# Kernel tuning notes

Hardware: AMD Instinct MI355X
Metric: run time of the kernel (lower is better)

Reference implementation:

```python
import jax, jax.numpy as jnp
import numpy as np

N_OSC = 256
N_LAYERS = 4
STEPS = 10
DT = 0.1
B = 1024
D_IN = 512
D_OUT = 128


def setup_inputs() -> dict:
    key = jax.random.key(0)
    ks = jax.random.split(key, 12)
    n = N_OSC

    def rn(k, shape, s=1.0):
        return jax.random.normal(k, shape, jnp.float32) * s

    K = rn(ks[0], (N_LAYERS, n, n), 0.1)
    K = (K + jnp.swapaxes(K, -1, -2)) / 2  # symmetric init as in torch
    return {
        "x": rn(ks[1], (B, D_IN)),
        "enc_W1": rn(ks[2], (D_IN, 2 * n), 0.02), "enc_b1": jnp.zeros((2 * n,), jnp.float32),
        "enc_W2": rn(ks[3], (2 * n, n), 0.02), "enc_b2": jnp.zeros((n,), jnp.float32),
        "K": K,
        "omega": rn(ks[4], (N_LAYERS, n), 0.1),
        "K_global": jnp.full((N_LAYERS,), 0.5, jnp.float32),
        "op_strength": jnp.full((6,), 0.5, jnp.float32),
        "exchange_logits": rn(ks[5], (n, n), 0.1),
        "catalyze_freq": rn(ks[6], (n,), 0.1),
        "sel_W1": rn(ks[7], (n + 2, 64), 0.05), "sel_b1": jnp.zeros((64,), jnp.float32),
        "sel_W2": rn(ks[8], (64, 6), 0.05), "sel_b2": jnp.zeros((6,), jnp.float32),
        "dec_W1": rn(ks[9], (2 * n, 2 * D_OUT), 0.02), "dec_b1": jnp.zeros((2 * D_OUT,), jnp.float32),
        "dec_W2": rn(ks[10], (2 * D_OUT, D_OUT), 0.02), "dec_b2": jnp.zeros((D_OUT,), jnp.float32),
        "z_momentum": jnp.float32(0.1),
        "z_decay": jnp.float32(0.05),
    }


def _kuramoto_layer(theta, K, omega, K_global):
    n = theta.shape[-1]

    def step(th, _):
        diff = th[:, None, :] - th[:, :, None]          # [B, i, j] = theta_j - theta_i
        coupling = jnp.sum(K * jnp.sin(diff), axis=-1)  # reduce over j -> [B, n]
        th_new = th + DT * (omega + (K_global / n) * coupling)
        th_new = jnp.arctan2(jnp.sin(th_new), jnp.cos(th_new))  # wrap to (-pi, pi]
        return th_new, None

    theta, _ = jax.lax.scan(jax.checkpoint(step), theta, None, length=STEPS)
    cm = jnp.mean(jnp.cos(theta), axis=-1)
    sm = jnp.mean(jnp.sin(theta), axis=-1)
    return theta, jnp.sqrt(cm * cm + sm * sm)  # Kuramoto order parameter r


def _soft_permutation(logits):
    P = logits
    for _ in range(5):  # Sinkhorn normalization in log space
        P = P - jax.nn.logsumexp(P, axis=-1, keepdims=True)
        P = P - jax.nn.logsumexp(P, axis=-2, keepdims=True)
    return jnp.exp(P)


def _forward(x, enc_W1, enc_b1, enc_W2, enc_b2, K, omega, K_global,
             op_strength, exchange_logits, catalyze_freq,
             sel_W1, sel_b1, sel_W2, sel_b2, dec_W1, dec_b1, dec_W2, dec_b2,
             z_momentum, z_decay):
    n = N_OSC
    # input encoding -> initial phases in (-pi, pi)
    h = jax.nn.gelu(x @ enc_W1 + enc_b1, approximate=False)
    theta = jnp.tanh(h @ enc_W2 + enc_b2) * jnp.pi

    z = jnp.float32(0.1)
    P = _soft_permutation(exchange_logits)
    k_mult = jnp.float32(1.0)              # AMPLIFY/CONTAIN carry to next layer
    om_add = jnp.zeros((n,), theta.dtype)  # CATALYZE carry to next layer

    for li in range(N_LAYERS):
        theta, r = _kuramoto_layer(theta, K[li] * k_mult, omega[li] + om_add, K_global[li])
        # z-coordinate attractor update: dz = mom*(r_mean - z) - decay*(z - 0.5)
        dz = z_momentum * (jnp.mean(r) - z) - z_decay * (z - 0.5)
        z = jnp.clip(z + 0.01 * dz, 0.0, 1.0)
        # APL operator selection from [theta, coherence, z]
        feat = jnp.concatenate(
            [theta, r[:, None], jnp.broadcast_to(z, (theta.shape[0], 1))], axis=-1)
        logits = jax.nn.gelu(feat @ sel_W1 + sel_b1, approximate=False) @ sel_W2 + sel_b2
        op = jnp.argmax(jnp.mean(logits, axis=0))
        strength = op_strength[op] * r[:, None]  # coherence-modulated strength
        sm_ = jnp.mean(strength)
        # apply operator: phase mods now, K/omega mods carried into next layer
        noise = jax.random.normal(jax.random.fold_in(jax.random.key(42), li),
                                  theta.shape, theta.dtype)
        theta = jnp.where(op == 3, theta @ P,                                # EXCHANGE
                          jnp.where(op == 4, theta + noise * strength * 0.2,  # INHIBIT
                                    theta))
        k_mult = jnp.where(op == 1, 1.0 + sm_ * 0.5,        # AMPLIFY
                           jnp.where(op == 2, 1.0 - sm_ * 0.3, 1.0))  # CONTAIN
        om_add = jnp.where(op == 5, catalyze_freq * sm_,    # CATALYZE
                           jnp.zeros_like(catalyze_freq))

    # decode from (cos, sin) phase embedding
    emb = jnp.concatenate([jnp.cos(theta), jnp.sin(theta)], axis=-1)  # [B, 2n]
    out = jax.nn.gelu(emb @ dec_W1 + dec_b1, approximate=False) @ dec_W2 + dec_b2
    return out


def reference(x, enc_W1, enc_b1, enc_W2, enc_b2, K, omega, K_global,
              op_strength, exchange_logits, catalyze_freq,
              sel_W1, sel_b1, sel_W2, sel_b2, dec_W1, dec_b1, dec_W2, dec_b2,
              z_momentum, z_decay):
    return _forward(x, enc_W1, enc_b1, enc_W2, enc_b2, K, omega, K_global,
                    op_strength, exchange_logits, catalyze_freq,
                    sel_W1, sel_b1, sel_W2, sel_b2, dec_W1, dec_b1, dec_W2, dec_b2,
                    z_momentum, z_decay)
```

## Files before the change

### kernel.cpp

```cpp
#include <hip/hip_runtime.h>
#include <hip/hip_fp16.h>
#include <math.h>

#define DT_F 0.1f

#define SC_Z     0
#define SC_RMEAN 1
#define SC_KMULT 2
#define SC_OP    3
#define SC_OPSTR 4
#define SC_SM    5

typedef __attribute__((ext_vector_type(8))) short short8;
typedef __attribute__((ext_vector_type(4))) float f32x4;


__device__ __forceinline__ float gelu_f(float x) {
    return 0.5f * x * (1.0f + erff(x * 0.7071067811865475f));
}

__device__ __forceinline__ unsigned short f2bf_rne(float f) {
    union { float f; unsigned u; } v; v.f = f;
    unsigned x = v.u;
    unsigned r = x + 0x7fffu + ((x >> 16) & 1u);
    return (unsigned short)(r >> 16);
}

__device__ __forceinline__ unsigned rotl32(unsigned v, int d) {
    return (v << d) | (v >> (32 - d));
}

__device__ __forceinline__ void threefry2x32(unsigned k0, unsigned k1,
                                             unsigned x0, unsigned x1,
                                             unsigned& o0, unsigned& o1) {
    unsigned k2 = k0 ^ k1 ^ 0x1BD11BDAu;
    x0 += k0; x1 += k1;
    const int r0[4] = {13, 15, 26, 6};
    const int r1[4] = {17, 29, 16, 24};
#pragma unroll
    for (int g = 0; g < 5; ++g) {
        const int* R = (g & 1) ? r1 : r0;
#pragma unroll
        for (int q = 0; q < 4; ++q) { x0 += x1; x1 = rotl32(x1, R[q]); x1 ^= x0; }
        unsigned a, b;
        switch (g) {
            case 0:  a = k1; b = k2 + 1u; break;
            case 1:  a = k2; b = k0 + 2u; break;
            case 2:  a = k0; b = k1 + 3u; break;
            case 3:  a = k1; b = k2 + 4u; break;
            default: a = k2; b = k0 + 5u; break;
        }
        x0 += a; x1 += b;
    }
    o0 = x0; o1 = x1;
}

__device__ __forceinline__ float erfinv_xla(float x) {
    float w = -log1pf(-x * x);
    float p;
    if (w < 5.0f) {
        w -= 2.5f;
        p = 2.81022636e-08f;
        p = fmaf(p, w, 3.43273939e-07f);
        p = fmaf(p, w, -3.5233877e-06f);
        p = fmaf(p, w, -4.39150654e-06f);
        p = fmaf(p, w, 0.00021858087f);
        p = fmaf(p, w, -0.00125372503f);
        p = fmaf(p, w, -0.00417768164f);
        p = fmaf(p, w, 0.246640727f);
        p = fmaf(p, w, 1.50140941f);
    } else {
        w = sqrtf(w) - 3.0f;
        p = -0.000200214257f;
        p = fmaf(p, w, 0.000100950558f);
        p = fmaf(p, w, 0.00134934322f);
        p = fmaf(p, w, -0.00367342844f);
        p = fmaf(p, w, 0.00573950773f);
        p = fmaf(p, w, -0.0076224613f);
        p = fmaf(p, w, 0.00943887047f);
        p = fmaf(p, w, 1.00167406f);
        p = fmaf(p, w, 2.83297682f);
    }
    return p * x;
}

__device__ __forceinline__ float jax_normal_elem(unsigned fk0, unsigned fk1, unsigned flat) {
    const unsigned HALF = 131072u;
    unsigned idx = (flat < HALF) ? flat : (flat - HALF);
    unsigned o0, o1;
    threefry2x32(fk0, fk1, idx, idx + HALF, o0, o1);
    unsigned bits = (flat < HALF) ? o0 : o1;
    float f = __uint_as_float((bits >> 9) | 0x3F800000u) - 1.0f;
    const float LO = __uint_as_float(0xBF7FFFFFu);
    float u = fmaxf(LO, fmaf(f, 2.0f, LO));
    return 1.41421356237f * erfinv_xla(u);
}


__global__ __launch_bounds__(256) void prep_wt_kernel(
    const float* __restrict__ W1, const float* __restrict__ W2,
    const float* __restrict__ W3, const float* __restrict__ W4,
    unsigned short* __restrict__ T1, unsigned short* __restrict__ T2,
    unsigned short* __restrict__ T3, unsigned short* __restrict__ T4)
{
    __shared__ float tile[64][65];
    int b = blockIdx.x;
    const float* W; unsigned short* T; int K, N, kt, nt;
    if (b < 64)       { W = W1; T = T1; K = 512; N = 512; kt = b >> 3; nt = b & 7; }
    else if (b < 96)  { b -= 64;  W = W2; T = T2; K = 512; N = 256; kt = b >> 2; nt = b & 3; }
    else if (b < 128) { b -= 96;  W = W3; T = T3; K = 512; N = 256; kt = b >> 2; nt = b & 3; }
    else              { b -= 128; W = W4; T = T4; K = 256; N = 128; kt = b >> 1; nt = b & 1; }
    const int k0 = kt * 64, n0 = nt * 64;
    const int t = threadIdx.x;

#pragma unroll
    for (int i = 0; i < 4; ++i) {
        int r = (t >> 4) + i * 16;
        int c = (t & 15) * 4;
        float4 v = *reinterpret_cast<const float4*>(&W[(k0 + r) * N + n0 + c]);
        tile[r][c] = v.x; tile[r][c + 1] = v.y; tile[r][c + 2] = v.z; tile[r][c + 3] = v.w;
    }
    __syncthreads();
#pragma unroll
    for (int i = 0; i < 4; ++i) {
        int nn = (t >> 4) + i * 16;
        int kc = (t & 15) * 4;
        ushort4 o;
        o.x = f2bf_rne(tile[kc + 0][nn]);
        o.y = f2bf_rne(tile[kc + 1][nn]);
        o.z = f2bf_rne(tile[kc + 2][nn]);
        o.w = f2bf_rne(tile[kc + 3][nn]);
        *reinterpret_cast<ushort4*>(&T[(n0 + nn) * K + k0 + kc]) = o;
    }
}


template <int ACT, int KF, bool EMB>
__global__ __launch_bounds__(256) void gemm_mfma_kernel(
    const float* __restrict__ A,
    const unsigned short* __restrict__ Wt,
    const float* __restrict__ bias,
    float* __restrict__ C, int N)
{
    constexpr int STR = KF + 8;
    __shared__ __align__(16) unsigned short A_s[64 * STR];
    __shared__ __align__(16) unsigned short B_s[64 * STR];
    const int tid = threadIdx.x;
    const int m_base = blockIdx.y * 64;
    const int n_base = blockIdx.x * 64;

    {
        constexpr int ITERS = 64 * KF / 2048;
#pragma unroll
        for (int c = 0; c < ITERS; ++c) {
            const int f = c * 2048 + tid * 8;
            const int row = f / KF, k = f % KF;
            float4 a0, a1;
            if (EMB) {
                const int kk = k & 255;
                a0 = *reinterpret_cast<const float4*>(&A[(m_base + row) * 256 + kk]);
                a1 = *reinterpret_cast<const float4*>(&A[(m_base + row) * 256 + kk + 4]);
                if (k < 256) {
                    a0.x = __cosf(a0.x); a0.y = __cosf(a0.y); a0.z = __cosf(a0.z); a0.w = __cosf(a0.w);
                    a1.x = __cosf(a1.x); a1.y = __cosf(a1.y); a1.z = __cosf(a1.z); a1.w = __cosf(a1.w);
                } else {
                    a0.x = __sinf(a0.x); a0.y = __sinf(a0.y); a0.z = __sinf(a0.z); a0.w = __sinf(a0.w);
                    a1.x = __sinf(a1.x); a1.y = __sinf(a1.y); a1.z = __sinf(a1.z); a1.w = __sinf(a1.w);
                }
            } else {
                a0 = *reinterpret_cast<const float4*>(&A[(m_base + row) * KF + k]);
                a1 = *reinterpret_cast<const float4*>(&A[(m_base + row) * KF + k + 4]);
            }
            short8 v;
            v[0] = (short)f2bf_rne(a0.x); v[1] = (short)f2bf_rne(a0.y);
            v[2] = (short)f2bf_rne(a0.z); v[3] = (short)f2bf_rne(a0.w);
            v[4] = (short)f2bf_rne(a1.x); v[5] = (short)f2bf_rne(a1.y);
            v[6] = (short)f2bf_rne(a1.z); v[7] = (short)f2bf_rne(a1.w);
            *reinterpret_cast<short8*>(&A_s[row * STR + k]) = v;
        }
    }
    {
        constexpr int ITERS = 64 * KF / 2048;
#pragma unroll
        for (int c = 0; c < ITERS; ++c) {
            const int f = c * 2048 + tid * 8;
            const int n = f / KF, k = f % KF;
            short8 v = *reinterpret_cast<const short8*>(&Wt[(n_base + n) * KF + k]);
            *reinterpret_cast<short8*>(&B_s[n * STR + k]) = v;
        }
    }
    __syncthreads();

    const int l = tid & 63, w = tid >> 6;
    const int lo = l & 15, hi = l >> 4;

    f32x4 acc0 = {0.f, 0.f, 0.f, 0.f};
    f32x4 acc1 = {0.f, 0.f, 0.f, 0.f};
    f32x4 acc2 = {0.f, 0.f, 0.f, 0.f};
    f32x4 acc3 = {0.f, 0.f, 0.f, 0.f};
#pragma unroll
    for (int kc = 0; kc < KF / 32; ++kc) {
        short8 af = *reinterpret_cast<const short8*>(&A_s[(w * 16 + lo) * STR + kc * 32 + hi * 8]);
        short8 b0 = *reinterpret_cast<const short8*>(&B_s[(0 * 16 + lo) * STR + kc * 32 + hi * 8]);
        short8 b1 = *reinterpret_cast<const short8*>(&B_s[(1 * 16 + lo) * STR + kc * 32 + hi * 8]);
        short8 b2 = *reinterpret_cast<const short8*>(&B_s[(2 * 16 + lo) * STR + kc * 32 + hi * 8]);
        short8 b3 = *reinterpret_cast<const short8*>(&B_s[(3 * 16 + lo) * STR + kc * 32 + hi * 8]);
        acc0 = __builtin_amdgcn_mfma_f32_16x16x32_bf16(af, b0, acc0, 0, 0, 0);
        acc1 = __builtin_amdgcn_mfma_f32_16x16x32_bf16(af, b1, acc1, 0, 0, 0);
        acc2 = __builtin_amdgcn_mfma_f32_16x16x32_bf16(af, b2, acc2, 0, 0, 0);
        acc3 = __builtin_amdgcn_mfma_f32_16x16x32_bf16(af, b3, acc3, 0, 0, 0);
    }

#pragma unroll
    for (int nf = 0; nf < 4; ++nf) {
        const f32x4 a = (nf == 0) ? acc0 : (nf == 1) ? acc1 : (nf == 2) ? acc2 : acc3;
        const int n = n_base + nf * 16 + lo;
        const float bv = bias[n];
#pragma unroll
        for (int q = 0; q < 4; ++q) {
            const int m = m_base + w * 16 + hi * 4 + q;
            float v = a[q] + bv;
            if (ACT == 1) v = gelu_f(v);
            else if (ACT == 2) v = tanhf(v) * 3.14159274101257324f;
            C[m * N + n] = v;
        }
    }
}


__global__ __launch_bounds__(1024) void sinkhorn_kernel(const float* __restrict__ logits,
                                                        float* __restrict__ P,
                                                        float* __restrict__ scal,
                                                        float* __restrict__ om_add) {
    __shared__ __align__(16) __half Eh[256][260];
    __shared__ float a[256], b[256];
    __shared__ float part[8][256];
    const int t = threadIdx.x;

    if (t < 8) {
        float val = 0.0f;
        if (t == SC_Z) val = 0.1f;
        if (t == SC_KMULT) val = 1.0f;
        scal[t] = val;
    }
    if (t < 256) { om_add[t] = 0.0f; b[t] = 1.0f; }

    {
        const int r = t >> 2, c0 = (t & 3) * 64;
#pragma unroll
        for (int j = 0; j < 64; j += 4) {
            float4 x4 = *reinterpret_cast<const float4*>(&logits[r * 256 + c0 + j]);
            __half2 h01 = __floats2half2_rn(__expf(x4.x), __expf(x4.y));
            __half2 h23 = __floats2half2_rn(__expf(x4.z), __expf(x4.w));
            *reinterpret_cast<__half2*>(&Eh[r][c0 + j])     = h01;
            *reinterpret_cast<__half2*>(&Eh[r][c0 + j + 2]) = h23;
        }
    }
    __syncthreads();

    for (int it = 0; it < 5; ++it) {
        {
            const int i = t & 255, q = t >> 8;
            float s0 = 0.f, s1 = 0.f, s2 = 0.f, s3 = 0.f;
#pragma unroll
            for (int j0 = 0; j0 < 64; j0 += 4) {
                float2 e4 = *reinterpret_cast<const float2*>(&Eh[i][q * 64 + j0]);
                const __half2* hp = reinterpret_cast<const __half2*>(&e4);
                float2 f01 = __half22float2(hp[0]);
                float2 f23 = __half22float2(hp[1]);
                float4 bv = *reinterpret_cast<const float4*>(&b[q * 64 + j0]);
                s0 = fmaf(f01.x, bv.x, s0);
                s1 = fmaf(f01.y, bv.y, s1);
                s2 = fmaf(f23.x, bv.z, s2);
                s3 = fmaf(f23.y, bv.w, s3);
            }
            part[q][i] = (s0 + s1) + (s2 + s3);
        }
        __syncthreads();
        if (t < 256) a[t] = 1.0f / (part[0][t] + part[1][t] + part[2][t] + part[3][t]);
        __syncthreads();
        {
            const int jp = t & 127, seg = t >> 7;
            float s0 = 0.f, s1 = 0.f;
#pragma unroll
            for (int i0 = 0; i0 < 32; i0 += 4) {
                float4 av = *reinterpret_cast<const float4*>(&a[seg * 32 + i0]);
                __half2 e0 = *reinterpret_cast<const __half2*>(&Eh[seg * 32 + i0 + 0][2 * jp]);
                __half2 e1 = *reinterpret_cast<const __half2*>(&Eh[seg * 32 + i0 + 1][2 * jp]);
                __half2 e2 = *reinterpret_cast<const __half2*>(&Eh[seg * 32 + i0 + 2][2 * jp]);
                __half2 e3 = *reinterpret_cast<const __half2*>(&Eh[seg * 32 + i0 + 3][2 * jp]);
                float2 f0 = __half22float2(e0), f1 = __half22float2(e1);
                float2 f2 = __half22float2(e2), f3 = __half22float2(e3);
                s0 = fmaf(f0.x, av.x, s0); s1 = fmaf(f0.y, av.x, s1);
                s0 = fmaf(f1.x, av.y, s0); s1 = fmaf(f1.y, av.y, s1);
                s0 = fmaf(f2.x, av.z, s0); s1 = fmaf(f2.y, av.z, s1);
                s0 = fmaf(f3.x, av.w, s0); s1 = fmaf(f3.y, av.w, s1);
            }
            part[seg][2 * jp]     = s0;
            part[seg][2 * jp + 1] = s1;
        }
        __syncthreads();
        if (t < 256) {
            float s = ((part[0][t] + part[1][t]) + (part[2][t] + part[3][t]))
                    + ((part[4][t] + part[5][t]) + (part[6][t] + part[7][t]));
            b[t] = 1.0f / s;
        }
        __syncthreads();
    }

    {
        const int r = t >> 2, c0 = (t & 3) * 64;
        const float ar = a[r];
#pragma unroll
        for (int j = 0; j < 64; j += 4) {
            float2 e4 = *reinterpret_cast<const float2*>(&Eh[r][c0 + j]);
            const __half2* hp = reinterpret_cast<const __half2*>(&e4);
            float2 f01 = __half22float2(hp[0]);
            float2 f23 = __half22float2(hp[1]);
            float4 bv = *reinterpret_cast<const float4*>(&b[c0 + j]);
            float4 o;
            o.x = f01.x * ar * bv.x;
            o.y = f01.y * ar * bv.y;
            o.z = f23.x * ar * bv.z;
            o.w = f23.y * ar * bv.w;
            *reinterpret_cast<float4*>(&P[r * 256 + c0 + j]) = o;
        }
    }
}


__global__ __launch_bounds__(512) void kuramoto_mfma_kernel(
    float* __restrict__ theta,
    const float* __restrict__ Kl,
    const float* __restrict__ omega_l,
    const float* __restrict__ Kg_p,
    const float* __restrict__ scal,
    const float* __restrict__ om_add,
    float* __restrict__ r_out,
    float* __restrict__ rpart,
    const float* __restrict__ P,
    int li)
{
    __shared__ __align__(16) unsigned short s_lds[16][264];
    __shared__ __align__(16) unsigned short c_lds[16][264];
    __shared__ __align__(16) float th_lds[16][260];
    __shared__ float rp_s[16][128];
    __shared__ float rp_c[16][128];
    __shared__ float red_s[16][32];
    __shared__ float red_c[16][32];
    __shared__ float rloc[16];

    const int tid = threadIdx.x;
    const int l  = tid & 63;
    const int w  = tid >> 6;
    const int lo = l & 15;
    const int hi = l >> 4;
    const int cb = w * 32;
    const int r0 = blockIdx.x * 16;

    const float gk = Kg_p[0] * (1.0f / 256.0f) * scal[SC_KMULT];
    const int op_prev = (int)scal[SC_OP];

    {
        const int row = tid >> 5;
        const int c0 = (tid & 31) * 8;
        float4 a = *reinterpret_cast<const float4*>(&theta[(r0 + row) * 256 + c0]);
        float4 b = *reinterpret_cast<const float4*>(&theta[(r0 + row) * 256 + c0 + 4]);
        *reinterpret_cast<float4*>(&th_lds[row][c0])     = a;
        *reinterpret_cast<float4*>(&th_lds[row][c0 + 4]) = b;
    }

    short8 kfrag[8][2];
#pragma unroll
    for (int nf = 0; nf < 2; ++nf) {
        const int col = cb + nf * 16 + lo;
        const float* krow = Kl + col * 256;
#pragma unroll
        for (int ks = 0; ks < 8; ++ks) {
            const int kb = ks * 32 + hi * 8;
            float4 k0 = *reinterpret_cast<const float4*>(&krow[kb]);
            float4 k1 = *reinterpret_cast<const float4*>(&krow[kb + 4]);
            short8 f;
            f[0] = (short)f2bf_rne(k0.x); f[1] = (short)f2bf_rne(k0.y);
            f[2] = (short)f2bf_rne(k0.z); f[3] = (short)f2bf_rne(k0.w);
            f[4] = (short)f2bf_rne(k1.x); f[5] = (short)f2bf_rne(k1.y);
            f[6] = (short)f2bf_rne(k1.z); f[7] = (short)f2bf_rne(k1.w);
            kfrag[ks][nf] = f;
        }
    }
    __syncthreads();

    float t[2][4];
    if (op_prev == 3) {
        float acc[2][4] = {};
        for (int j = 0; j < 256; ++j) {
            float p0 = P[j * 256 + cb + lo];
            float p1 = P[j * 256 + cb + 16 + lo];
#pragma unroll
            for (int q = 0; q < 4; ++q) {
                float tv = th_lds[hi * 4 + q][j];
                acc[0][q] = fmaf(tv, p0, acc[0][q]);
                acc[1][q] = fmaf(tv, p1, acc[1][q]);
            }
        }
#pragma unroll
        for (int nf = 0; nf < 2; ++nf)
#pragma unroll
            for (int q = 0; q < 4; ++q) t[nf][q] = acc[nf][q];
    } else {
#pragma unroll
        for (int nf = 0; nf < 2; ++nf)
#pragma unroll
            for (int q = 0; q < 4; ++q)
                t[nf][q] = th_lds[hi * 4 + q][cb + nf * 16 + lo];
        if (op_prev == 4) {
            unsigned fk0, fk1;
            threefry2x32(0u, 42u, 0u, (unsigned)(li - 1), fk0, fk1);
            const float opv = scal[SC_OPSTR];
#pragma unroll
            for (int nf = 0; nf < 2; ++nf)
#pragma unroll
                for (int q = 0; q < 4; ++q) {
                    const int row = hi * 4 + q;
                    const int col = cb + nf * 16 + lo;
                    unsigned flat = (unsigned)((r0 + row) * 256 + col);
                    float nz = jax_normal_elem(fk0, fk1, flat);
                    t[nf][q] += nz * opv * r_out[r0 + row] * 0.2f;
                }
        }
    }

    float si[2][4], ci[2][4];
    float om[2];
#pragma unroll
    for (int nf = 0; nf < 2; ++nf) {
        const int col = cb + nf * 16 + lo;
        om[nf] = omega_l[col] + om_add[col];
#pragma unroll
        for (int q = 0; q < 4; ++q) {
            const int row = hi * 4 + q;
            float sv, cv;
            __sincosf(t[nf][q], &sv, &cv);
            si[nf][q] = sv; ci[nf][q] = cv;
            s_lds[row][col] = f2bf_rne(sv);
            c_lds[row][col] = f2bf_rne(cv);
        }
    }
    __syncthreads();

    for (int s = 0; s < 10; ++s) {
        f32x4 accS0 = {0.f, 0.f, 0.f, 0.f};
        f32x4 accS1 = {0.f, 0.f, 0.f, 0.f};
        f32x4 accC0 = {0.f, 0.f, 0.f, 0.f};
        f32x4 accC1 = {0.f, 0.f, 0.f, 0.f};
#pragma unroll
        for (int ks = 0; ks < 8; ++ks) {
            short8 aS = *reinterpret_cast<const short8*>(&s_lds[lo][ks * 32 + hi * 8]);
            short8 aC = *reinterpret_cast<const short8*>(&c_lds[lo][ks * 32 + hi * 8]);
            accS0 = __builtin_amdgcn_mfma_f32_16x16x32_bf16(aS, kfrag[ks][0], accS0, 0, 0, 0);
            accS1 = __builtin_amdgcn_mfma_f32_16x16x32_bf16(aS, kfrag[ks][1], accS1, 0, 0, 0);
            accC0 = __builtin_amdgcn_mfma_f32_16x16x32_bf16(aC, kfrag[ks][0], accC0, 0, 0, 0);
            accC1 = __builtin_amdgcn_mfma_f32_16x16x32_bf16(aC, kfrag[ks][1], accC1, 0, 0, 0);
        }
        __syncthreads();

#pragma unroll
        for (int nf = 0; nf < 2; ++nf) {
#pragma unroll
            for (int q = 0; q < 4; ++q) {
                float aS = (nf == 0) ? accS0[q] : accS1[q];
                float aC = (nf == 0) ? accC0[q] : accC1[q];
                float coup = ci[nf][q] * aS - si[nf][q] * aC;
                float tn = t[nf][q] + DT_F * (om[nf] + gk * coup);
                t[nf][q] = tn;
                float sv, cv;
                __sincosf(tn, &sv, &cv);
                si[nf][q] = sv; ci[nf][q] = cv;
                const int row = hi * 4 + q;
                const int col = cb + nf * 16 + lo;
                s_lds[row][col] = f2bf_rne(sv);
                c_lds[row][col] = f2bf_rne(cv);
            }
        }
        __syncthreads();
    }

#pragma unroll
    for (int q = 0; q < 4; ++q) {
        const int row = hi * 4 + q;
        rp_s[row][w * 16 + lo] = si[0][q] + si[1][q];
        rp_c[row][w * 16 + lo] = ci[0][q] + ci[1][q];
    }
#pragma unroll
    for (int nf = 0; nf < 2; ++nf) {
#pragma unroll
        for (int q = 0; q < 4; ++q) {
            const int row = hi * 4 + q;
            const int col = cb + nf * 16 + lo;
            theta[(r0 + row) * 256 + col] = atan2f(si[nf][q], ci[nf][q]);
        }
    }
    __syncthreads();

    {
        const int row = tid >> 5;
        const int i = tid & 31;
        float ssum = rp_s[row][i] + rp_s[row][i + 32] + rp_s[row][i + 64] + rp_s[row][i + 96];
        float csum = rp_c[row][i] + rp_c[row][i + 32] + rp_c[row][i + 64] + rp_c[row][i + 96];
        red_s[row][i] = ssum;
        red_c[row][i] = csum;
        __syncthreads();
#pragma unroll
        for (int off = 16; off > 0; off >>= 1) {
            if (i < off) {
                red_s[row][i] += red_s[row][i + off];
                red_c[row][i] += red_c[row][i + off];
            }
            __syncthreads();
        }
        if (i == 0) {
            float sm = red_s[row][0] * (1.0f / 256.0f);
            float cm = red_c[row][0] * (1.0f / 256.0f);
            float rv = sqrtf(cm * cm + sm * sm);
            r_out[r0 + row] = rv;
            rloc[row] = rv;
        }
        __syncthreads();
        if (tid == 0) {
            float s = 0.0f;
#pragma unroll
            for (int rr = 0; rr < 16; ++rr) s += rloc[rr];
            rpart[blockIdx.x] = s;
        }
    }
}


__global__ __launch_bounds__(256) void sel_partial_kernel(const float* __restrict__ theta,
                                                          const float* __restrict__ rbuf,
                                                          const float* __restrict__ rpart,
                                                          const float* __restrict__ scal,
                                                          const float* __restrict__ W1,
                                                          const float* __restrict__ b1,
                                                          const float* __restrict__ zm_p,
                                                          const float* __restrict__ zd_p,
                                                          float* __restrict__ partial) {
    __shared__ float Wt[64][261];
    __shared__ float th_s[4][256];
    __shared__ float gl[4][64];
    __shared__ float s_z;
    const int t = threadIdx.x;
    const int h = t & 63;
    const int rr = t >> 6;
    const int blk = blockIdx.x;

    if (t < 64) {
        float s = rpart[t];
#pragma unroll
        for (int off = 32; off > 0; off >>= 1) s += __shfl_down(s, off);
        if (t == 0) {
            float rmean = s * (1.0f / 1024.0f);
            float zp = scal[SC_Z];
            float dz = (*zm_p) * (rmean - zp) - (*zd_p) * (zp - 0.5f);
            float zn = zp + 0.01f * dz;
            s_z = fminf(fmaxf(zn, 0.0f), 1.0f);
        }
    }

    for (int idx = t; idx < 258 * 64; idx += 256)
        Wt[idx & 63][idx >> 6] = W1[idx];

    {
        const int c0 = h * 4;
        float4 v = *reinterpret_cast<const float4*>(&theta[(blk * 4 + rr) * 256 + c0]);
        *reinterpret_cast<float4*>(&th_s[rr][c0]) = v;
    }
    __syncthreads();

    const float z = s_z;
    float d0 = 0.f, d1 = 0.f, d2 = 0.f, d3 = 0.f;
#pragma unroll 4
    for (int k0 = 0; k0 < 256; k0 += 4) {
        float4 tv = *reinterpret_cast<const float4*>(&th_s[rr][k0]);
        d0 = fmaf(tv.x, Wt[h][k0 + 0], d0);
        d1 = fmaf(tv.y, Wt[h][k0 + 1], d1);
        d2 = fmaf(tv.z, Wt[h][k0 + 2], d2);
        d3 = fmaf(tv.w, Wt[h][k0 + 3], d3);
    }
    float full = (d0 + d1) + (d2 + d3) + b1[h]
               + rbuf[blk * 4 + rr] * Wt[h][256] + z * Wt[h][257];
    gl[rr][h] = gelu_f(full);
    __syncthreads();
    if (t < 64) partial[blk * 64 + t] = ((gl[0][t] + gl[1][t]) + gl[2][t]) + gl[3][t];
}


__global__ __launch_bounds__(256) void op_finalize_kernel(const float* __restrict__ partial,
                                                          const float* __restrict__ W2,
                                                          const float* __restrict__ b2,
                                                          const float* __restrict__ opstr,
                                                          const float* __restrict__ cf,
                                                          const float* __restrict__ rpart,
                                                          const float* __restrict__ zm_p,
                                                          const float* __restrict__ zd_p,
                                                          float* __restrict__ scal,
                                                          float* __restrict__ om_add) {
    __shared__ float red[4][64];
    __shared__ float hbar[64];
    __shared__ float lg[6];
    __shared__ float s_rmean;
    __shared__ float s_sm;
    __shared__ int s_op;
    const int t = threadIdx.x;
    const int h = t & 63;
    const int q = t >> 6;

    if (t < 64) {
        float s = rpart[t];
#pragma unroll
        for (int off = 32; off > 0; off >>= 1) s += __shfl_down(s, off);
        if (t == 0) s_rmean = s * (1.0f / 1024.0f);
    }

    float s = 0.0f;
#pragma unroll 8
    for (int blk = q * 64; blk < q * 64 + 64; ++blk) s += partial[blk * 64 + h];
    red[q][h] = s;
    __syncthreads();
    if (t < 64) hbar[t] = (red[0][t] + red[1][t] + red[2][t] + red[3][t]) * (1.0f / 1024.0f);
    __syncthreads();
    if (t < 6) {
        float l = b2[t];
        for (int hh = 0; hh < 64; ++hh) l = fmaf(hbar[hh], W2[hh * 6 + t], l);
        lg[t] = l;
    }
    __syncthreads();
    if (t == 0) {
        float rmean = s_rmean;
        float zp = scal[SC_Z];
        float dz = (*zm_p) * (rmean - zp) - (*zd_p) * (zp - 0.5f);
        float zn = zp + 0.01f * dz;
        zn = fminf(fmaxf(zn, 0.0f), 1.0f);
        scal[SC_Z] = zn;
        scal[SC_RMEAN] = rmean;

        float best = -1e30f;
        int op = 0;
#pragma unroll
        for (int o = 0; o < 6; ++o) {
            if (lg[o] > best) { best = lg[o]; op = o; }
        }
        float sm = opstr[op] * rmean;
        scal[SC_OP] = (float)op;
        scal[SC_OPSTR] = opstr[op];
        scal[SC_SM] = sm;
        scal[SC_KMULT] = (op == 1) ? (1.0f + sm * 0.5f)
                        : (op == 2) ? (1.0f - sm * 0.3f) : 1.0f;
        s_sm = sm;
        s_op = op;
    }
    __syncthreads();
    om_add[t] = (s_op == 5) ? cf[t] * s_sm : 0.0f;
}


__global__ __launch_bounds__(256) void apply_op_kernel(float* __restrict__ theta,
                                                       const float* __restrict__ P,
                                                       const float* __restrict__ r,
                                                       const float* __restrict__ scal,
                                                       int li) {
    __shared__ float th[8][256];
    const int op = (int)scal[SC_OP];
    const int i = threadIdx.x;
    const int b0 = blockIdx.x * 8;

    if (op == 3) {
#pragma unroll
        for (int rr = 0; rr < 8; ++rr) th[rr][i] = theta[(b0 + rr) * 256 + i];
        __syncthreads();
        float acc[8] = {0.f, 0.f, 0.f, 0.f, 0.f, 0.f, 0.f, 0.f};
        for (int j = 0; j < 256; ++j) {
            float pv = P[j * 256 + i];
#pragma unroll
            for (int rr = 0; rr < 8; ++rr) acc[rr] = fmaf(th[rr][j], pv, acc[rr]);
        }
#pragma unroll
        for (int rr = 0; rr < 8; ++rr) theta[(b0 + rr) * 256 + i] = acc[rr];
    } else if (op == 4) {
        unsigned fk0, fk1;
        threefry2x32(0u, 42u, 0u, (unsigned)li, fk0, fk1);
        const float opv = scal[SC_OPSTR];
#pragma unroll
        for (int rr = 0; rr < 8; ++rr) {
            int b = b0 + rr;
            unsigned flat = (unsigned)(b * 256 + i);
            float nz = jax_normal_elem(fk0, fk1, flat);
            float strength = opv * r[b];
            theta[b * 256 + i] += nz * strength * 0.2f;
        }
    }
}


extern "C" void kernel_launch(void* const* d_in, const int* in_sizes, int n_in,
                              void* d_out, int out_size, void* d_ws, size_t ws_size,
                              hipStream_t stream) {
    const float* x     = (const float*)d_in[0];
    const float* eW1   = (const float*)d_in[1];
    const float* eb1   = (const float*)d_in[2];
    const float* eW2   = (const float*)d_in[3];
    const float* eb2   = (const float*)d_in[4];
    const float* K     = (const float*)d_in[5];
    const float* omega = (const float*)d_in[6];
    const float* Kg    = (const float*)d_in[7];
    const float* opstr = (const float*)d_in[8];
    const float* exlog = (const float*)d_in[9];
    const float* cfreq = (const float*)d_in[10];
    const float* sW1   = (const float*)d_in[11];
    const float* sb1   = (const float*)d_in[12];
    const float* sW2   = (const float*)d_in[13];
    const float* sb2   = (const float*)d_in[14];
    const float* dW1   = (const float*)d_in[15];
    const float* db1   = (const float*)d_in[16];
    const float* dW2   = (const float*)d_in[17];
    const float* db2   = (const float*)d_in[18];
    const float* zm    = (const float*)d_in[19];
    const float* zd    = (const float*)d_in[20];
    float* out = (float*)d_out;

    float* ws      = (float*)d_ws;
    float* P       = ws;
    float* theta   = P + 65536;
    float* h       = theta + 262144;
    float* dh      = h + 524288;
    float* rbuf    = dh + 262144;
    float* scal    = rbuf + 1024;
    float* om_add  = scal + 8;
    float* partial = om_add + 256;
    float* rpart   = partial + 16384;
    unsigned short* W1t = (unsigned short*)(rpart + 64);
    unsigned short* W2t = (unsigned short*)(rpart + 64 + 131072);
    unsigned short* W3t = (unsigned short*)(rpart + 64 + 131072 + 65536);
    unsigned short* W4t = (unsigned short*)(rpart + 64 + 131072 + 65536 + 65536);

    prep_wt_kernel<<<136, 256, 0, stream>>>(eW1, eW2, dW1, dW2, W1t, W2t, W3t, W4t);
    sinkhorn_kernel<<<1, 1024, 0, stream>>>(exlog, P, scal, om_add);

    gemm_mfma_kernel<1, 512, false><<<dim3(8, 16), 256, 0, stream>>>(x, W1t, eb1, h, 512);
    gemm_mfma_kernel<2, 512, false><<<dim3(4, 16), 256, 0, stream>>>(h, W2t, eb2, theta, 256);

    for (int li = 0; li < 4; ++li) {
        kuramoto_mfma_kernel<<<64, 512, 0, stream>>>(theta, K + li * 65536, omega + li * 256,
                                                     Kg + li, scal, om_add, rbuf, rpart, P, li);
        sel_partial_kernel<<<256, 256, 0, stream>>>(theta, rbuf, rpart, scal, sW1, sb1,
                                                    zm, zd, partial);
        op_finalize_kernel<<<1, 256, 0, stream>>>(partial, sW2, sb2, opstr, cfreq, rpart,
                                                  zm, zd, scal, om_add);
    }

    apply_op_kernel<<<128, 256, 0, stream>>>(theta, P, rbuf, scal, 3);
    gemm_mfma_kernel<1, 512, true><<<dim3(4, 16), 256, 0, stream>>>(theta, W3t, db1, dh, 256);
    gemm_mfma_kernel<0, 256, false><<<dim3(2, 16), 256, 0, stream>>>(dh, W4t, db2, out, 128);

    (void)in_sizes; (void)n_in; (void)out_size; (void)ws_size;
}
```

Baseline: 207.0 us.

## Widen Kuramoto blocks, double-buffer phase LDS, fuse op finalize via last-block atomic

The Kuramoto kernel now runs 1024 threads per block, with each wave owning one 16-column tile instead of two. The sin/cos LDS tiles are double-buffered, which removes one barrier per integration step, and the row reduction of the order parameter now uses wave shuffles. The separate single-block op_finalize launch is folded into the selector kernel through an atomic counter, so the last block to finish does the finalize and the kernel count per layer drops. This adds threadfence and atomic overhead, and it relies on counters that sinkhorn_kernel zeroes once per forward call.

```diff
diff --git a/kernel.cpp b/kernel.cpp
--- a/kernel.cpp
+++ b/kernel.cpp
@@ -231,7 +231,8 @@
 __global__ __launch_bounds__(1024) void sinkhorn_kernel(const float* __restrict__ logits,
                                                         float* __restrict__ P,
                                                         float* __restrict__ scal,
-                                                        float* __restrict__ om_add) {
+                                                        float* __restrict__ om_add,
+                                                        unsigned* __restrict__ counters) {
     __shared__ __align__(16) __half Eh[256][260];
     __shared__ float a[256], b[256];
     __shared__ float part[8][256];
@@ -243,6 +244,7 @@
         if (t == SC_KMULT) val = 1.0f;
         scal[t] = val;
     }
+    if (t >= 8 && t < 12) counters[t - 8] = 0u;
     if (t < 256) { om_add[t] = 0.0f; b[t] = 1.0f; }
 
     {
@@ -329,7 +331,7 @@
 }
 
 
-__global__ __launch_bounds__(512) void kuramoto_mfma_kernel(
+__global__ __launch_bounds__(1024, 4) void kuramoto_mfma_kernel(
     float* __restrict__ theta,
     const float* __restrict__ Kl,
     const float* __restrict__ omega_l,
@@ -341,13 +343,11 @@
     const float* __restrict__ P,
     int li)
 {
-    __shared__ __align__(16) unsigned short s_lds[16][264];
-    __shared__ __align__(16) unsigned short c_lds[16][264];
+    __shared__ __align__(16) unsigned short s_lds[2][16][264];
+    __shared__ __align__(16) unsigned short c_lds[2][16][264];
     __shared__ __align__(16) float th_lds[16][260];
-    __shared__ float rp_s[16][128];
-    __shared__ float rp_c[16][128];
-    __shared__ float red_s[16][32];
-    __shared__ float red_c[16][32];
+    __shared__ float rp_s[16][256];
+    __shared__ float rp_c[16][256];
     __shared__ float rloc[16];
 
     const int tid = threadIdx.x;
@@ -355,25 +355,21 @@
     const int w  = tid >> 6;
     const int lo = l & 15;
     const int hi = l >> 4;
-    const int cb = w * 32;
+    const int col = w * 16 + lo;
     const int r0 = blockIdx.x * 16;
 
     const float gk = Kg_p[0] * (1.0f / 256.0f) * scal[SC_KMULT];
     const int op_prev = (int)scal[SC_OP];
 
     {
-        const int row = tid >> 5;
-        const int c0 = (tid & 31) * 8;
+        const int row = tid >> 6;
+        const int c0 = (tid & 63) * 4;
         float4 a = *reinterpret_cast<const float4*>(&theta[(r0 + row) * 256 + c0]);
-        float4 b = *reinterpret_cast<const float4*>(&theta[(r0 + row) * 256 + c0 + 4]);
-        *reinterpret_cast<float4*>(&th_lds[row][c0])     = a;
-        *reinterpret_cast<float4*>(&th_lds[row][c0 + 4]) = b;
-    }
-
-    short8 kfrag[8][2];
-#pragma unroll
-    for (int nf = 0; nf < 2; ++nf) {
-        const int col = cb + nf * 16 + lo;
+        *reinterpret_cast<float4*>(&th_lds[row][c0]) = a;
+    }
+
+    short8 kfrag[8];
+    {
         const float* krow = Kl + col * 256;
 #pragma unroll
         for (int ks = 0; ks < 8; ++ks) {
@@ -385,170 +381,133 @@
             f[2] = (short)f2bf_rne(k0.z); f[3] = (short)f2bf_rne(k0.w);
             f[4] = (short)f2bf_rne(k1.x); f[5] = (short)f2bf_rne(k1.y);
             f[6] = (short)f2bf_rne(k1.z); f[7] = (short)f2bf_rne(k1.w);
-            kfrag[ks][nf] = f;
-        }
-    }
-    __syncthreads();
-
-    float t[2][4];
+            kfrag[ks] = f;
+        }
+    }
+    __syncthreads();
+
+    float t[4];
     if (op_prev == 3) {
-        float acc[2][4] = {};
+        float a0 = 0.f, a1 = 0.f, a2 = 0.f, a3 = 0.f;
         for (int j = 0; j < 256; ++j) {
-            float p0 = P[j * 256 + cb + lo];
-            float p1 = P[j * 256 + cb + 16 + lo];
-#pragma unroll
-            for (int q = 0; q < 4; ++q) {
-                float tv = th_lds[hi * 4 + q][j];
-                acc[0][q] = fmaf(tv, p0, acc[0][q]);
-                acc[1][q] = fmaf(tv, p1, acc[1][q]);
-            }
-        }
-#pragma unroll
-        for (int nf = 0; nf < 2; ++nf)
-#pragma unroll
-            for (int q = 0; q < 4; ++q) t[nf][q] = acc[nf][q];
+            float pv = P[j * 256 + col];
+            a0 = fmaf(th_lds[hi * 4 + 0][j], pv, a0);
+            a1 = fmaf(th_lds[hi * 4 + 1][j], pv, a1);
+            a2 = fmaf(th_lds[hi * 4 + 2][j], pv, a2);
+            a3 = fmaf(th_lds[hi * 4 + 3][j], pv, a3);
+        }
+        t[0] = a0; t[1] = a1; t[2] = a2; t[3] = a3;
     } else {
 #pragma unroll
-        for (int nf = 0; nf < 2; ++nf)
-#pragma unroll
-            for (int q = 0; q < 4; ++q)
-                t[nf][q] = th_lds[hi * 4 + q][cb + nf * 16 + lo];
+        for (int q = 0; q < 4; ++q) t[q] = th_lds[hi * 4 + q][col];
         if (op_prev == 4) {
             unsigned fk0, fk1;
             threefry2x32(0u, 42u, 0u, (unsigned)(li - 1), fk0, fk1);
             const float opv = scal[SC_OPSTR];
 #pragma unroll
-            for (int nf = 0; nf < 2; ++nf)
-#pragma unroll
-                for (int q = 0; q < 4; ++q) {
-                    const int row = hi * 4 + q;
-                    const int col = cb + nf * 16 + lo;
-                    unsigned flat = (unsigned)((r0 + row) * 256 + col);
-                    float nz = jax_normal_elem(fk0, fk1, flat);
-                    t[nf][q] += nz * opv * r_out[r0 + row] * 0.2f;
-                }
-        }
-    }
-
-    float si[2][4], ci[2][4];
-    float om[2];
-#pragma unroll
-    for (int nf = 0; nf < 2; ++nf) {
-        const int col = cb + nf * 16 + lo;
-        om[nf] = omega_l[col] + om_add[col];
+            for (int q = 0; q < 4; ++q) {
+                const int row = hi * 4 + q;
+                unsigned flat = (unsigned)((r0 + row) * 256 + col);
+                float nz = jax_normal_elem(fk0, fk1, flat);
+                t[q] += nz * opv * r_out[r0 + row] * 0.2f;
+            }
+        }
+    }
+
+    const float om = omega_l[col] + om_add[col];
+    float si[4], ci[4];
+#pragma unroll
+    for (int q = 0; q < 4; ++q) {
+        float sv, cv;
+        __sincosf(t[q], &sv, &cv);
+        si[q] = sv; ci[q] = cv;
+        s_lds[0][hi * 4 + q][col] = f2bf_rne(sv);
+        c_lds[0][hi * 4 + q][col] = f2bf_rne(cv);
+    }
+    __syncthreads();
+
+    int cur = 0;
+    for (int s = 0; s < 10; ++s) {
+        f32x4 accS = {0.f, 0.f, 0.f, 0.f};
+        f32x4 accC = {0.f, 0.f, 0.f, 0.f};
+#pragma unroll
+        for (int ks = 0; ks < 8; ++ks) {
+            short8 aS = *reinterpret_cast<const short8*>(&s_lds[cur][lo][ks * 32 + hi * 8]);
+            short8 aC = *reinterpret_cast<const short8*>(&c_lds[cur][lo][ks * 32 + hi * 8]);
+            accS = __builtin_amdgcn_mfma_f32_16x16x32_bf16(aS, kfrag[ks], accS, 0, 0, 0);
+            accC = __builtin_amdgcn_mfma_f32_16x16x32_bf16(aC, kfrag[ks], accC, 0, 0, 0);
+        }
+        const int nxt = cur ^ 1;
 #pragma unroll
         for (int q = 0; q < 4; ++q) {
-            const int row = hi * 4 + q;
+            float coup = ci[q] * accS[q] - si[q] * accC[q];
+            float tn = t[q] + DT_F * (om + gk * coup);
+            t[q] = tn;
             float sv, cv;
-            __sincosf(t[nf][q], &sv, &cv);
-            si[nf][q] = sv; ci[nf][q] = cv;
-            s_lds[row][col] = f2bf_rne(sv);
-            c_lds[row][col] = f2bf_rne(cv);
-        }
-    }
-    __syncthreads();
-
-    for (int s = 0; s < 10; ++s) {
-        f32x4 accS0 = {0.f, 0.f, 0.f, 0.f};
-        f32x4 accS1 = {0.f, 0.f, 0.f, 0.f};
-        f32x4 accC0 = {0.f, 0.f, 0.f, 0.f};
-        f32x4 accC1 = {0.f, 0.f, 0.f, 0.f};
-#pragma unroll
-        for (int ks = 0; ks < 8; ++ks) {
-            short8 aS = *reinterpret_cast<const short8*>(&s_lds[lo][ks * 32 + hi * 8]);
-            short8 aC = *reinterpret_cast<const short8*>(&c_lds[lo][ks * 32 + hi * 8]);
-            accS0 = __builtin_amdgcn_mfma_f32_16x16x32_bf16(aS, kfrag[ks][0], accS0, 0, 0, 0);
-            accS1 = __builtin_amdgcn_mfma_f32_16x16x32_bf16(aS, kfrag[ks][1], accS1, 0, 0, 0);
-            accC0 = __builtin_amdgcn_mfma_f32_16x16x32_bf16(aC, kfrag[ks][0], accC0, 0, 0, 0);
-            accC1 = __builtin_amdgcn_mfma_f32_16x16x32_bf16(aC, kfrag[ks][1], accC1, 0, 0, 0);
+            __sincosf(tn, &sv, &cv);
+            si[q] = sv; ci[q] = cv;
+            s_lds[nxt][hi * 4 + q][col] = f2bf_rne(sv);
+            c_lds[nxt][hi * 4 + q][col] = f2bf_rne(cv);
         }
         __syncthreads();
-
-#pragma unroll
-        for (int nf = 0; nf < 2; ++nf) {
-#pragma unroll
-            for (int q = 0; q < 4; ++q) {
-                float aS = (nf == 0) ? accS0[q] : accS1[q];
-                float aC = (nf == 0) ? accC0[q] : accC1[q];
-                float coup = ci[nf][q] * aS - si[nf][q] * aC;
-                float tn = t[nf][q] + DT_F * (om[nf] + gk * coup);
-                t[nf][q] = tn;
-                float sv, cv;
-                __sincosf(tn, &sv, &cv);
-                si[nf][q] = sv; ci[nf][q] = cv;
-                const int row = hi * 4 + q;
-                const int col = cb + nf * 16 + lo;
-                s_lds[row][col] = f2bf_rne(sv);
-                c_lds[row][col] = f2bf_rne(cv);
-            }
-        }
-        __syncthreads();
+        cur = nxt;
     }
 
 #pragma unroll
     for (int q = 0; q < 4; ++q) {
         const int row = hi * 4 + q;
-        rp_s[row][w * 16 + lo] = si[0][q] + si[1][q];
-        rp_c[row][w * 16 + lo] = ci[0][q] + ci[1][q];
-    }
-#pragma unroll
-    for (int nf = 0; nf < 2; ++nf) {
-#pragma unroll
-        for (int q = 0; q < 4; ++q) {
-            const int row = hi * 4 + q;
-            const int col = cb + nf * 16 + lo;
-            theta[(r0 + row) * 256 + col] = atan2f(si[nf][q], ci[nf][q]);
-        }
+        rp_s[row][col] = si[q];
+        rp_c[row][col] = ci[q];
+        theta[(r0 + row) * 256 + col] = atan2f(si[q], ci[q]);
     }
     __syncthreads();
 
     {
-        const int row = tid >> 5;
-        const int i = tid & 31;
-        float ssum = rp_s[row][i] + rp_s[row][i + 32] + rp_s[row][i + 64] + rp_s[row][i + 96];
-        float csum = rp_c[row][i] + rp_c[row][i + 32] + rp_c[row][i + 64] + rp_c[row][i + 96];
-        red_s[row][i] = ssum;
-        red_c[row][i] = csum;
-        __syncthreads();
-#pragma unroll
-        for (int off = 16; off > 0; off >>= 1) {
-            if (i < off) {
-                red_s[row][i] += red_s[row][i + off];
-                red_c[row][i] += red_c[row][i + off];
-            }
-            __syncthreads();
-        }
-        if (i == 0) {
-            float sm = red_s[row][0] * (1.0f / 256.0f);
-            float cm = red_c[row][0] * (1.0f / 256.0f);
+        float s = rp_s[w][l] + rp_s[w][l + 64] + rp_s[w][l + 128] + rp_s[w][l + 192];
+        float c = rp_c[w][l] + rp_c[w][l + 64] + rp_c[w][l + 128] + rp_c[w][l + 192];
+#pragma unroll
+        for (int off = 32; off > 0; off >>= 1) {
+            s += __shfl_down(s, off);
+            c += __shfl_down(c, off);
+        }
+        if (l == 0) {
+            float sm = s * (1.0f / 256.0f);
+            float cm = c * (1.0f / 256.0f);
             float rv = sqrtf(cm * cm + sm * sm);
-            r_out[r0 + row] = rv;
-            rloc[row] = rv;
+            r_out[r0 + w] = rv;
+            rloc[w] = rv;
         }
         __syncthreads();
         if (tid == 0) {
-            float s = 0.0f;
-#pragma unroll
-            for (int rr = 0; rr < 16; ++rr) s += rloc[rr];
-            rpart[blockIdx.x] = s;
-        }
-    }
-}
-
-
-__global__ __launch_bounds__(256) void sel_partial_kernel(const float* __restrict__ theta,
-                                                          const float* __restrict__ rbuf,
-                                                          const float* __restrict__ rpart,
-                                                          const float* __restrict__ scal,
-                                                          const float* __restrict__ W1,
-                                                          const float* __restrict__ b1,
-                                                          const float* __restrict__ zm_p,
-                                                          const float* __restrict__ zd_p,
-                                                          float* __restrict__ partial) {
+            float acc = 0.0f;
+#pragma unroll
+            for (int rr = 0; rr < 16; ++rr) acc += rloc[rr];
+            rpart[blockIdx.x] = acc;
+        }
+    }
+}
+
+
+__global__ __launch_bounds__(256) void sel_op_kernel(const float* __restrict__ theta,
+                                                     const float* __restrict__ rbuf,
+                                                     const float* __restrict__ rpart,
+                                                     float* __restrict__ scal,
+                                                     const float* __restrict__ W1,
+                                                     const float* __restrict__ b1,
+                                                     const float* __restrict__ W2,
+                                                     const float* __restrict__ b2,
+                                                     const float* __restrict__ opstr,
+                                                     const float* __restrict__ cf,
+                                                     const float* __restrict__ zm_p,
+                                                     const float* __restrict__ zd_p,
+                                                     float* __restrict__ partial,
+                                                     unsigned* __restrict__ counter,
+                                                     float* __restrict__ om_add) {
     __shared__ float Wt[64][261];
     __shared__ float th_s[4][256];
     __shared__ float gl[4][64];
-    __shared__ float s_z;
+    __shared__ float s_z, s_rmean;
+    __shared__ unsigned s_done;
     const int t = threadIdx.x;
     const int h = t & 63;
     const int rr = t >> 6;
@@ -560,6 +519,7 @@
         for (int off = 32; off > 0; off >>= 1) s += __shfl_down(s, off);
         if (t == 0) {
             float rmean = s * (1.0f / 1024.0f);
+            s_rmean = rmean;
             float zp = scal[SC_Z];
             float dz = (*zm_p) * (rmean - zp) - (*zd_p) * (zp - 0.5f);
             float zn = zp + 0.01f * dz;
@@ -592,65 +552,43 @@
     gl[rr][h] = gelu_f(full);
     __syncthreads();
     if (t < 64) partial[blk * 64 + t] = ((gl[0][t] + gl[1][t]) + gl[2][t]) + gl[3][t];
-}
-
-
-__global__ __launch_bounds__(256) void op_finalize_kernel(const float* __restrict__ partial,
-                                                          const float* __restrict__ W2,
-                                                          const float* __restrict__ b2,
-                                                          const float* __restrict__ opstr,
-                                                          const float* __restrict__ cf,
-                                                          const float* __restrict__ rpart,
-                                                          const float* __restrict__ zm_p,
-                                                          const float* __restrict__ zd_p,
-                                                          float* __restrict__ scal,
-                                                          float* __restrict__ om_add) {
+
+    __threadfence();
+    if (t == 0) s_done = atomicAdd(counter, 1u);
+    __syncthreads();
+    if (s_done != 255) return;
+    __threadfence();
+
     __shared__ float red[4][64];
     __shared__ float hbar[64];
     __shared__ float lg[6];
-    __shared__ float s_rmean;
     __shared__ float s_sm;
     __shared__ int s_op;
-    const int t = threadIdx.x;
-    const int h = t & 63;
     const int q = t >> 6;
-
-    if (t < 64) {
-        float s = rpart[t];
-#pragma unroll
-        for (int off = 32; off > 0; off >>= 1) s += __shfl_down(s, off);
-        if (t == 0) s_rmean = s * (1.0f / 1024.0f);
-    }
 
     float s = 0.0f;
 #pragma unroll 8
-    for (int blk = q * 64; blk < q * 64 + 64; ++blk) s += partial[blk * 64 + h];
+    for (int bb = q * 64; bb < q * 64 + 64; ++bb) s += partial[bb * 64 + h];
     red[q][h] = s;
     __syncthreads();
     if (t < 64) hbar[t] = (red[0][t] + red[1][t] + red[2][t] + red[3][t]) * (1.0f / 1024.0f);
     __syncthreads();
     if (t < 6) {
-        float l = b2[t];
-        for (int hh = 0; hh < 64; ++hh) l = fmaf(hbar[hh], W2[hh * 6 + t], l);
-        lg[t] = l;
+        float lv = b2[t];
+        for (int hh = 0; hh < 64; ++hh) lv = fmaf(hbar[hh], W2[hh * 6 + t], lv);
+        lg[t] = lv;
     }
     __syncthreads();
     if (t == 0) {
-        float rmean = s_rmean;
-        float zp = scal[SC_Z];
-        float dz = (*zm_p) * (rmean - zp) - (*zd_p) * (zp - 0.5f);
-        float zn = zp + 0.01f * dz;
-        zn = fminf(fmaxf(zn, 0.0f), 1.0f);
-        scal[SC_Z] = zn;
-        scal[SC_RMEAN] = rmean;
-
+        scal[SC_Z] = s_z;
+        scal[SC_RMEAN] = s_rmean;
         float best = -1e30f;
         int op = 0;
 #pragma unroll
         for (int o = 0; o < 6; ++o) {
             if (lg[o] > best) { best = lg[o]; op = o; }
         }
-        float sm = opstr[op] * rmean;
+        float sm = opstr[op] * s_rmean;
         scal[SC_OP] = (float)op;
         scal[SC_OPSTR] = opstr[op];
         scal[SC_SM] = sm;
@@ -742,20 +680,20 @@
     unsigned short* W2t = (unsigned short*)(rpart + 64 + 131072);
     unsigned short* W3t = (unsigned short*)(rpart + 64 + 131072 + 65536);
     unsigned short* W4t = (unsigned short*)(rpart + 64 + 131072 + 65536 + 65536);
+    unsigned* counters  = (unsigned*)(rpart + 64 + 131072 + 65536 + 65536 + 16384);
 
     prep_wt_kernel<<<136, 256, 0, stream>>>(eW1, eW2, dW1, dW2, W1t, W2t, W3t, W4t);
-    sinkhorn_kernel<<<1, 1024, 0, stream>>>(exlog, P, scal, om_add);
+    sinkhorn_kernel<<<1, 1024, 0, stream>>>(exlog, P, scal, om_add, counters);
 
     gemm_mfma_kernel<1, 512, false><<<dim3(8, 16), 256, 0, stream>>>(x, W1t, eb1, h, 512);
     gemm_mfma_kernel<2, 512, false><<<dim3(4, 16), 256, 0, stream>>>(h, W2t, eb2, theta, 256);
 
     for (int li = 0; li < 4; ++li) {
-        kuramoto_mfma_kernel<<<64, 512, 0, stream>>>(theta, K + li * 65536, omega + li * 256,
-                                                     Kg + li, scal, om_add, rbuf, rpart, P, li);
-        sel_partial_kernel<<<256, 256, 0, stream>>>(theta, rbuf, rpart, scal, sW1, sb1,
-                                                    zm, zd, partial);
-        op_finalize_kernel<<<1, 256, 0, stream>>>(partial, sW2, sb2, opstr, cfreq, rpart,
-                                                  zm, zd, scal, om_add);
+        kuramoto_mfma_kernel<<<64, 1024, 0, stream>>>(theta, K + li * 65536, omega + li * 256,
+                                                      Kg + li, scal, om_add, rbuf, rpart, P, li);
+        sel_op_kernel<<<256, 256, 0, stream>>>(theta, rbuf, rpart, scal, sW1, sb1, sW2, sb2,
+                                               opstr, cfreq, zm, zd, partial,
+                                               counters + li, om_add);
     }
 
     apply_op_kernel<<<128, 256, 0, stream>>>(theta, P, rbuf, scal, 3);
```

Result: slower. 274.7 us (+32.7%).
